# Kernel optimization log

Hardware: AMD Instinct MI355X
Metric: run time of the kernel (lower is better)

The kernel has to match this reference:

```python
import jax, jax.numpy as jnp
import numpy as np

BS, N, XC, K, YS = 64, 1024, 1024, 256, 768

def setup_inputs() -> dict:
    key = jax.random.key(0)
    ks = jax.random.split(key, 5)
    return {
        "x": jax.random.normal(ks[0], (BS, N, XC), dtype=jnp.float32),
        "y": jax.random.normal(ks[1], (BS, YS), dtype=jnp.float32),
        "W_ch": jax.random.normal(ks[2], (K, XC), dtype=jnp.float32) * 0.02,
        "b_ch": jax.random.normal(ks[3], (K,), dtype=jnp.float32) * 0.02,
        "W_y": jax.random.normal(ks[4], (K, YS), dtype=jnp.float32) * 0.02,
    }

def reference(x, y, W_ch, b_ch, W_y):
    # y_k: [bs, k] (no bias)
    y_k = jnp.einsum('bs,ks->bk', y, W_y)
    # channel affine on every spatial position, batched: [bs, n, k]
    x_k = jnp.einsum('bnc,kc->bnk', x, W_ch) + b_ch
    # add per-sample y_k (broadcast over spatial dim), tanh, softmax over k
    z = jnp.tanh(x_k + y_k[:, None, :])
    attn = jax.nn.softmax(z, axis=-1)
    # torch.cat over dim=0 of per-sample [n, k] blocks -> [bs*n, k]
    return attn.reshape(-1, attn.shape[-1])
```

## Files before the change

kernel.cpp:

```cpp
#include <hip/hip_runtime.h>


#define XC    1024
#define KOUT  256
#define NT    16
#define LDSZ  16384

typedef float        f32x4_t  __attribute__((ext_vector_type(4)));
typedef unsigned int u32x4_t  __attribute__((ext_vector_type(4)));
typedef unsigned int u32x2_t  __attribute__((ext_vector_type(2)));
typedef __bf16       bf16x8_t __attribute__((ext_vector_type(8)));

__device__ __forceinline__ unsigned short f2bf(float f) {
  unsigned int u = __float_as_uint(f);
  u += 0x7fffu + ((u >> 16) & 1u);
  return (unsigned short)(u >> 16);
}

__device__ __forceinline__ float fast_tanh(float v) {
  float e = __expf(2.0f * v);
  return 1.0f - 2.0f / (e + 1.0f);
}

#define LGKM_BARRIER() do {                                  \
    asm volatile("s_waitcnt lgkmcnt(0)" ::: "memory");       \
    __builtin_amdgcn_s_barrier();                            \
    __builtin_amdgcn_sched_barrier(0);                       \
  } while (0)

__global__ void prep_kernel(const float* __restrict__ Wch,
                            const float* __restrict__ y,
                            const float* __restrict__ Wy,
                            const float* __restrict__ bch,
                            unsigned short* __restrict__ wbf,
                            float* __restrict__ biasws) {
  if (blockIdx.x < 256) {
    const int k = blockIdx.x;
    const int u = threadIdx.x;
    f32x4_t v = ((const f32x4_t*)(Wch + k * XC))[u];
    const int c0   = u << 2;
    const int t    = c0 >> 6;
    const int ch   = (c0 & 63) >> 3;
    const int kk   = ch >> 2;
    const int lg   = ch & 3;
    const int half = (c0 >> 2) & 1;
    const int wv   = k >> 6;
    const int ni   = (k >> 4) & 3;
    const int lr   = k & 15;
    const int lane = (lg << 4) | lr;
    unsigned int lo = (unsigned int)f2bf(v.x) | ((unsigned int)f2bf(v.y) << 16);
    unsigned int hi = (unsigned int)f2bf(v.z) | ((unsigned int)f2bf(v.w) << 16);
    char* p = (char*)wbf +
              ((size_t)((((t << 2) + wv) * 2 + kk) * 4 + ni) << 10) +
              (lane << 4) + (half << 3);
    *(u32x2_t*)p = (u32x2_t){lo, hi};
  } else {
    __shared__ __align__(16) float ys[768];
    const int b = blockIdx.x - 256;
    const int k = threadIdx.x;
    for (int i = k; i < 768; i += 256) ys[i] = y[b * 768 + i];
    __syncthreads();
    const f32x4_t* w4 = (const f32x4_t*)(Wy + k * 768);
    const f32x4_t* y4 = (const f32x4_t*)ys;
    float s = 0.f;
#pragma unroll 8
    for (int i = 0; i < 192; ++i) {
      f32x4_t w = w4[i], a = y4[i];
      s = fmaf(w.x, a.x, s); s = fmaf(w.y, a.y, s);
      s = fmaf(w.z, a.z, s); s = fmaf(w.w, a.w, s);
    }
    biasws[b * 256 + k] = s + bch[k];
  }
}

__global__ __launch_bounds__(256, 2) void fused_kernel(
    const float* __restrict__ x, const unsigned short* __restrict__ wbf,
    const float* __restrict__ bias, float* __restrict__ out) {
  __shared__ __align__(16) unsigned char smem[LDSZ];
  const int tid = threadIdx.x;
  const int l   = tid & 63;
  const int wv  = tid >> 6;
  const int lr  = l & 15;
  const int lg  = l >> 4;
  const int m0  = blockIdx.x << 6;
  const int bidx = m0 >> 10;
  const int rr  = tid >> 4;
  const int c4  = tid & 15;
  const int t0  = blockIdx.x & 15;

  f32x4_t acc[4][4];
#pragma unroll
  for (int i = 0; i < 4; ++i)
#pragma unroll
    for (int j = 0; j < 4; ++j) acc[i][j] = (f32x4_t){0.f, 0.f, 0.f, 0.f};

  const float* xb = x + (size_t)m0 * XC + (size_t)rr * XC + (c4 << 2);
  const char* wsrc = (const char*)wbf + (wv << 13) + (l << 4);
  f32x4_t av0[4], av1[4], av2[4];
  bf16x8_t bfrA[8], bfrB[8];

#define LOADA(dst, tt) do {                                                  \
    _Pragma("unroll")                                                        \
    for (int j = 0; j < 4; ++j)                                              \
      dst[j] = *(const f32x4_t*)(xb + (size_t)(j << 4) * XC + ((tt) << 6));  \
  } while (0)

#define LOADB(dst, tt) do {                                                  \
    const char* g = wsrc + (size_t)(tt) * 32768;                             \
    _Pragma("unroll")                                                        \
    for (int f = 0; f < 8; ++f)                                              \
      dst[f] = __builtin_bit_cast(bf16x8_t, *(const u32x4_t*)(g + (f << 10)));\
  } while (0)

#define WRITEA(src, buf) do {                                                \
    _Pragma("unroll")                                                        \
    for (int j = 0; j < 4; ++j) {                                            \
      const int row = (j << 4) + rr;                                         \
      unsigned int lo = (unsigned int)f2bf(src[j].x) |                       \
                        ((unsigned int)f2bf(src[j].y) << 16);                \
      unsigned int hi = (unsigned int)f2bf(src[j].z) |                       \
                        ((unsigned int)f2bf(src[j].w) << 16);                \
      char* p = (char*)smem + ((buf) << 13) + row * 128 +                    \
                (((c4 >> 1) ^ (row & 7)) << 4) + ((c4 & 1) << 3);            \
      *(u32x2_t*)p = (u32x2_t){lo, hi};                                      \
    }                                                                        \
  } while (0)

#define COMPUTE(buf, bsrc) do {                                              \
    const u32x4_t* aB = (const u32x4_t*)(smem + ((buf) << 13));              \
    _Pragma("unroll")                                                        \
    for (int kk = 0; kk < 2; ++kk) {                                         \
      const int cs = ((kk << 2) | lg) ^ (lr & 7);                            \
      bf16x8_t afr[4];                                                       \
      _Pragma("unroll")                                                      \
      for (int mi = 0; mi < 4; ++mi)                                         \
        afr[mi] = __builtin_bit_cast(bf16x8_t, aB[(((mi << 4) + lr) << 3) + cs]);\
      _Pragma("unroll")                                                      \
      for (int mi = 0; mi < 4; ++mi)                                         \
        _Pragma("unroll")                                                    \
        for (int nj = 0; nj < 4; ++nj)                                       \
          acc[mi][nj] = __builtin_amdgcn_mfma_f32_16x16x32_bf16(             \
              afr[mi], bsrc[(kk << 2) | nj], acc[mi][nj], 0, 0, 0);          \
    }                                                                        \
  } while (0)

#define STEP(s, bC, bN, aW, aL, bufC, bufN) do {                             \
    if ((s) + 1 < NT) LOADB(bN, (((s) + 1 + t0) & 15));                      \
    if ((s) + 3 < NT) LOADA(aL, (((s) + 3 + t0) & 15));                      \
    COMPUTE(bufC, bC);                                                       \
    if ((s) + 1 < NT) { WRITEA(aW, bufN); LGKM_BARRIER(); }                  \
  } while (0)

  LOADB(bfrA, t0);
  LOADA(av0, t0);
  LOADA(av1, (t0 + 1) & 15);
  LOADA(av2, (t0 + 2) & 15);
  WRITEA(av0, 0);
  LGKM_BARRIER();

  STEP( 0, bfrA, bfrB, av1, av0, 0, 1);
  STEP( 1, bfrB, bfrA, av2, av1, 1, 0);
  STEP( 2, bfrA, bfrB, av0, av2, 0, 1);
  STEP( 3, bfrB, bfrA, av1, av0, 1, 0);
  STEP( 4, bfrA, bfrB, av2, av1, 0, 1);
  STEP( 5, bfrB, bfrA, av0, av2, 1, 0);
  STEP( 6, bfrA, bfrB, av1, av0, 0, 1);
  STEP( 7, bfrB, bfrA, av2, av1, 1, 0);
  STEP( 8, bfrA, bfrB, av0, av2, 0, 1);
  STEP( 9, bfrB, bfrA, av1, av0, 1, 0);
  STEP(10, bfrA, bfrB, av2, av1, 0, 1);
  STEP(11, bfrB, bfrA, av0, av2, 1, 0);
  STEP(12, bfrA, bfrB, av1, av0, 0, 1);
  STEP(13, bfrB, bfrA, av2, av1, 1, 0);
  STEP(14, bfrA, bfrB, av0, av2, 0, 1);
  STEP(15, bfrB, bfrA, av1, av0, 1, 0);

  __syncthreads();

#undef LOADA
#undef LOADB
#undef WRITEA
#undef COMPUTE
#undef STEP

  float* wred    = (float*)smem;
  float* rowstat = (float*)(smem + 1024);

  float brow[4];
#pragma unroll
  for (int ni = 0; ni < 4; ++ni)
    brow[ni] = bias[(bidx << 8) + (wv << 6) + (ni << 4) + lr];

#pragma unroll
  for (int mi = 0; mi < 4; ++mi)
#pragma unroll
    for (int ni = 0; ni < 4; ++ni)
#pragma unroll
      for (int r = 0; r < 4; ++r)
        acc[mi][ni][r] = fast_tanh(acc[mi][ni][r] + brow[ni]);

#pragma unroll
  for (int mi = 0; mi < 4; ++mi)
#pragma unroll
    for (int r = 0; r < 4; ++r) {
      float m = fmaxf(fmaxf(acc[mi][0][r], acc[mi][1][r]),
                      fmaxf(acc[mi][2][r], acc[mi][3][r]));
      m = fmaxf(m, __shfl_xor(m, 1));
      m = fmaxf(m, __shfl_xor(m, 2));
      m = fmaxf(m, __shfl_xor(m, 4));
      m = fmaxf(m, __shfl_xor(m, 8));
      if (lr == 0) wred[(wv << 6) + (mi << 4) + (lg << 2) + r] = m;
    }
  __syncthreads();
  if (tid < 64)
    rowstat[tid] = fmaxf(fmaxf(wred[tid], wred[64 + tid]),
                         fmaxf(wred[128 + tid], wred[192 + tid]));
  __syncthreads();

#pragma unroll
  for (int mi = 0; mi < 4; ++mi)
#pragma unroll
    for (int r = 0; r < 4; ++r) {
      const int row = (mi << 4) + (lg << 2) + r;
      const float m = rowstat[row];
      float s = 0.f;
#pragma unroll
      for (int ni = 0; ni < 4; ++ni) {
        float e = __expf(acc[mi][ni][r] - m);
        acc[mi][ni][r] = e;
        s += e;
      }
      s += __shfl_xor(s, 1);
      s += __shfl_xor(s, 2);
      s += __shfl_xor(s, 4);
      s += __shfl_xor(s, 8);
      if (lr == 0) wred[(wv << 6) + row] = s;
    }
  __syncthreads();
  if (tid < 64)
    rowstat[tid] = 1.0f / (wred[tid] + wred[64 + tid] +
                           wred[128 + tid] + wred[192 + tid]);
  __syncthreads();

#pragma unroll
  for (int mi = 0; mi < 4; ++mi)
#pragma unroll
    for (int r = 0; r < 4; ++r) {
      const int row = (mi << 4) + (lg << 2) + r;
      const float rinv = rowstat[row];
      float* orow = out + (size_t)(m0 + row) * KOUT + (wv << 6) + lr;
#pragma unroll
      for (int ni = 0; ni < 4; ++ni)
        orow[ni << 4] = acc[mi][ni][r] * rinv;
    }
}

extern "C" void kernel_launch(void* const* d_in, const int* in_sizes, int n_in,
                              void* d_out, int out_size, void* d_ws, size_t ws_size,
                              hipStream_t stream) {
  (void)in_sizes; (void)n_in; (void)out_size; (void)ws_size;
  const float* x   = (const float*)d_in[0];
  const float* y   = (const float*)d_in[1];
  const float* Wch = (const float*)d_in[2];
  const float* bch = (const float*)d_in[3];
  const float* Wy  = (const float*)d_in[4];
  float* out = (float*)d_out;
  unsigned short* wbf = (unsigned short*)d_ws;
  float* biasws = (float*)((char*)d_ws + 512 * 1024);

  hipLaunchKernelGGL(prep_kernel, dim3(320), dim3(256), 0, stream,
                     Wch, y, Wy, bch, wbf, biasws);
  hipLaunchKernelGGL(fused_kernel, dim3(1024), dim3(256), 0, stream,
                     x, wbf, biasws, out);
}
```

Before: 111.4 us.

## Process two row tiles per block, prefetching second tile during first

Halves the grid so each block computes two 64-row tiles back to back. The second tile's A and B loads are issued during the tail and epilogue of the first tile, which hides the pipeline fill latency. The bf16 conversion also moves to a cheaper pack with round-half-up instead of round-to-nearest-even. The cost is fewer blocks (512 on 256 CUs at 2 per CU), which may leave CUs underused, and higher register pressure from the prefetch held across the epilogue.

```diff
diff --git a/kernel.cpp b/kernel.cpp
--- a/kernel.cpp
+++ b/kernel.cpp
@@ -15,6 +15,12 @@
   unsigned int u = __float_as_uint(f);
   u += 0x7fffu + ((u >> 16) & 1u);
   return (unsigned short)(u >> 16);
+}
+
+__device__ __forceinline__ unsigned int pack2bf(float a, float b) {
+  unsigned int ua = __float_as_uint(a) + 0x8000u;
+  unsigned int ub = __float_as_uint(b) + 0x8000u;
+  return (ua >> 16) | (ub & 0xffff0000u);
 }
 
 __device__ __forceinline__ float fast_tanh(float v) {
@@ -82,27 +88,30 @@
   const int wv  = tid >> 6;
   const int lr  = l & 15;
   const int lg  = l >> 4;
-  const int m0  = blockIdx.x << 6;
-  const int bidx = m0 >> 10;
+  const int m0a = blockIdx.x << 6;
+  const int m0b = (blockIdx.x + 512) << 6;
   const int rr  = tid >> 4;
   const int c4  = tid & 15;
   const int t0  = blockIdx.x & 15;
 
   f32x4_t acc[4][4];
-#pragma unroll
-  for (int i = 0; i < 4; ++i)
-#pragma unroll
-    for (int j = 0; j < 4; ++j) acc[i][j] = (f32x4_t){0.f, 0.f, 0.f, 0.f};
-
-  const float* xb = x + (size_t)m0 * XC + (size_t)rr * XC + (c4 << 2);
+  const float* xb0 = x + (size_t)m0a * XC + (size_t)rr * XC + (c4 << 2);
+  const float* xb1 = x + (size_t)m0b * XC + (size_t)rr * XC + (c4 << 2);
   const char* wsrc = (const char*)wbf + (wv << 13) + (l << 4);
   f32x4_t av0[4], av1[4], av2[4];
   bf16x8_t bfrA[8], bfrB[8];
 
-#define LOADA(dst, tt) do {                                                  \
+#define ZERO_ACC() do {                                                      \
+    _Pragma("unroll")                                                        \
+    for (int i = 0; i < 4; ++i)                                              \
+      _Pragma("unroll")                                                      \
+      for (int j = 0; j < 4; ++j) acc[i][j] = (f32x4_t){0.f, 0.f, 0.f, 0.f}; \
+  } while (0)
+
+#define LOADA(dst, base, tt) do {                                            \
     _Pragma("unroll")                                                        \
     for (int j = 0; j < 4; ++j)                                              \
-      dst[j] = *(const f32x4_t*)(xb + (size_t)(j << 4) * XC + ((tt) << 6));  \
+      dst[j] = *(const f32x4_t*)((base) + (size_t)(j << 4) * XC + ((tt) << 6));\
   } while (0)
 
 #define LOADB(dst, tt) do {                                                  \
@@ -116,10 +125,8 @@
     _Pragma("unroll")                                                        \
     for (int j = 0; j < 4; ++j) {                                            \
       const int row = (j << 4) + rr;                                         \
-      unsigned int lo = (unsigned int)f2bf(src[j].x) |                       \
-                        ((unsigned int)f2bf(src[j].y) << 16);                \
-      unsigned int hi = (unsigned int)f2bf(src[j].z) |                       \
-                        ((unsigned int)f2bf(src[j].w) << 16);                \
+      unsigned int lo = pack2bf(src[j].x, src[j].y);                         \
+      unsigned int hi = pack2bf(src[j].z, src[j].w);                         \
       char* p = (char*)smem + ((buf) << 13) + row * 128 +                    \
                 (((c4 >> 1) ^ (row & 7)) << 4) + ((c4 & 1) << 3);            \
       *(u32x2_t*)p = (u32x2_t){lo, hi};                                      \
@@ -144,115 +151,158 @@
     }                                                                        \
   } while (0)
 
-#define STEP(s, bC, bN, aW, aL, bufC, bufN) do {                             \
-    if ((s) + 1 < NT) LOADB(bN, (((s) + 1 + t0) & 15));                      \
-    if ((s) + 3 < NT) LOADA(aL, (((s) + 3 + t0) & 15));                      \
-    COMPUTE(bufC, bC);                                                       \
-    if ((s) + 1 < NT) { WRITEA(aW, bufN); LGKM_BARRIER(); }                  \
-  } while (0)
-
+#define STEP(s, bC, bN, aW, aL, XB) do {                                     \
+    LOADB(bN, (((s) + 1 + t0) & 15));                                        \
+    LOADA(aL, XB, (((s) + 3 + t0) & 15));                                    \
+    COMPUTE((s) & 1, bC);                                                    \
+    WRITEA(aW, ((s) + 1) & 1);                                               \
+    LGKM_BARRIER();                                                          \
+  } while (0)
+
+#define EPILOGUE(M0V, BIDXV) do {                                            \
+    float* wred    = (float*)smem;                                           \
+    float* rowstat = (float*)(smem + 1024);                                  \
+    float brow[4];                                                           \
+    _Pragma("unroll")                                                        \
+    for (int ni = 0; ni < 4; ++ni)                                           \
+      brow[ni] = bias[((BIDXV) << 8) + (wv << 6) + (ni << 4) + lr];          \
+    _Pragma("unroll")                                                        \
+    for (int mi = 0; mi < 4; ++mi)                                           \
+      _Pragma("unroll")                                                      \
+      for (int ni = 0; ni < 4; ++ni)                                         \
+        _Pragma("unroll")                                                    \
+        for (int r = 0; r < 4; ++r)                                          \
+          acc[mi][ni][r] = fast_tanh(acc[mi][ni][r] + brow[ni]);             \
+    _Pragma("unroll")                                                        \
+    for (int mi = 0; mi < 4; ++mi)                                           \
+      _Pragma("unroll")                                                      \
+      for (int r = 0; r < 4; ++r) {                                          \
+        float m = fmaxf(fmaxf(acc[mi][0][r], acc[mi][1][r]),                 \
+                        fmaxf(acc[mi][2][r], acc[mi][3][r]));                \
+        m = fmaxf(m, __shfl_xor(m, 1));                                      \
+        m = fmaxf(m, __shfl_xor(m, 2));                                      \
+        m = fmaxf(m, __shfl_xor(m, 4));                                      \
+        m = fmaxf(m, __shfl_xor(m, 8));                                      \
+        if (lr == 0) wred[(wv << 6) + (mi << 4) + (lg << 2) + r] = m;        \
+      }                                                                      \
+    LGKM_BARRIER();                                                          \
+    if (tid < 64)                                                            \
+      rowstat[tid] = fmaxf(fmaxf(wred[tid], wred[64 + tid]),                 \
+                           fmaxf(wred[128 + tid], wred[192 + tid]));         \
+    LGKM_BARRIER();                                                          \
+    _Pragma("unroll")                                                        \
+    for (int mi = 0; mi < 4; ++mi)                                           \
+      _Pragma("unroll")                                                      \
+      for (int r = 0; r < 4; ++r) {                                          \
+        const int row = (mi << 4) + (lg << 2) + r;                           \
+        const float m = rowstat[row];                                        \
+        float s = 0.f;                                                       \
+        _Pragma("unroll")                                                    \
+        for (int ni = 0; ni < 4; ++ni) {                                     \
+          float e = __expf(acc[mi][ni][r] - m);                              \
+          acc[mi][ni][r] = e;                                                \
+          s += e;                                                            \
+        }                                                                    \
+        s += __shfl_xor(s, 1);                                               \
+        s += __shfl_xor(s, 2);                                               \
+        s += __shfl_xor(s, 4);                                               \
+        s += __shfl_xor(s, 8);                                               \
+        if (lr == 0) wred[(wv << 6) + row] = s;                              \
+      }                                                                      \
+    LGKM_BARRIER();                                                          \
+    if (tid < 64)                                                            \
+      rowstat[tid] = 1.0f / (wred[tid] + wred[64 + tid] +                    \
+                             wred[128 + tid] + wred[192 + tid]);             \
+    LGKM_BARRIER();                                                          \
+    _Pragma("unroll")                                                        \
+    for (int mi = 0; mi < 4; ++mi)                                           \
+      _Pragma("unroll")                                                      \
+      for (int r = 0; r < 4; ++r) {                                          \
+        const int row = (mi << 4) + (lg << 2) + r;                           \
+        const float rinv = rowstat[row];                                     \
+        float* orow = out + (size_t)((M0V) + row) * KOUT + (wv << 6) + lr;   \
+        _Pragma("unroll")                                                    \
+        for (int ni = 0; ni < 4; ++ni)                                       \
+          orow[ni << 4] = acc[mi][ni][r] * rinv;                             \
+      }                                                                      \
+  } while (0)
+
+  ZERO_ACC();
   LOADB(bfrA, t0);
-  LOADA(av0, t0);
-  LOADA(av1, (t0 + 1) & 15);
-  LOADA(av2, (t0 + 2) & 15);
+  LOADA(av0, xb0, t0);
+  LOADA(av1, xb0, (t0 + 1) & 15);
+  LOADA(av2, xb0, (t0 + 2) & 15);
   WRITEA(av0, 0);
   LGKM_BARRIER();
 
-  STEP( 0, bfrA, bfrB, av1, av0, 0, 1);
-  STEP( 1, bfrB, bfrA, av2, av1, 1, 0);
-  STEP( 2, bfrA, bfrB, av0, av2, 0, 1);
-  STEP( 3, bfrB, bfrA, av1, av0, 1, 0);
-  STEP( 4, bfrA, bfrB, av2, av1, 0, 1);
-  STEP( 5, bfrB, bfrA, av0, av2, 1, 0);
-  STEP( 6, bfrA, bfrB, av1, av0, 0, 1);
-  STEP( 7, bfrB, bfrA, av2, av1, 1, 0);
-  STEP( 8, bfrA, bfrB, av0, av2, 0, 1);
-  STEP( 9, bfrB, bfrA, av1, av0, 1, 0);
-  STEP(10, bfrA, bfrB, av2, av1, 0, 1);
-  STEP(11, bfrB, bfrA, av0, av2, 1, 0);
-  STEP(12, bfrA, bfrB, av1, av0, 0, 1);
-  STEP(13, bfrB, bfrA, av2, av1, 1, 0);
-  STEP(14, bfrA, bfrB, av0, av2, 0, 1);
-  STEP(15, bfrB, bfrA, av1, av0, 1, 0);
-
-  __syncthreads();
-
+  STEP( 0, bfrA, bfrB, av1, av0, xb0);
+  STEP( 1, bfrB, bfrA, av2, av1, xb0);
+  STEP( 2, bfrA, bfrB, av0, av2, xb0);
+  STEP( 3, bfrB, bfrA, av1, av0, xb0);
+  STEP( 4, bfrA, bfrB, av2, av1, xb0);
+  STEP( 5, bfrB, bfrA, av0, av2, xb0);
+  STEP( 6, bfrA, bfrB, av1, av0, xb0);
+  STEP( 7, bfrB, bfrA, av2, av1, xb0);
+  STEP( 8, bfrA, bfrB, av0, av2, xb0);
+  STEP( 9, bfrB, bfrA, av1, av0, xb0);
+  STEP(10, bfrA, bfrB, av2, av1, xb0);
+  STEP(11, bfrB, bfrA, av0, av2, xb0);
+  STEP(12, bfrA, bfrB, av1, av0, xb0);
+  LOADB(bfrA, (14 + t0) & 15);
+  LOADA(av1, xb1, t0);
+  COMPUTE(1, bfrB);
+  WRITEA(av2, 0);
+  LGKM_BARRIER();
+  LOADB(bfrB, (15 + t0) & 15);
+  LOADA(av2, xb1, (t0 + 1) & 15);
+  COMPUTE(0, bfrA);
+  WRITEA(av0, 1);
+  LGKM_BARRIER();
+  LOADB(bfrA, t0);
+  LOADA(av0, xb1, (t0 + 2) & 15);
+  COMPUTE(1, bfrB);
+  LGKM_BARRIER();
+
+  EPILOGUE(m0a, (m0a >> 10));
+  LGKM_BARRIER();
+
+  ZERO_ACC();
+  WRITEA(av1, 0);
+  LGKM_BARRIER();
+
+  STEP( 0, bfrA, bfrB, av2, av1, xb1);
+  STEP( 1, bfrB, bfrA, av0, av2, xb1);
+  STEP( 2, bfrA, bfrB, av1, av0, xb1);
+  STEP( 3, bfrB, bfrA, av2, av1, xb1);
+  STEP( 4, bfrA, bfrB, av0, av2, xb1);
+  STEP( 5, bfrB, bfrA, av1, av0, xb1);
+  STEP( 6, bfrA, bfrB, av2, av1, xb1);
+  STEP( 7, bfrB, bfrA, av0, av2, xb1);
+  STEP( 8, bfrA, bfrB, av1, av0, xb1);
+  STEP( 9, bfrB, bfrA, av2, av1, xb1);
+  STEP(10, bfrA, bfrB, av0, av2, xb1);
+  STEP(11, bfrB, bfrA, av1, av0, xb1);
+  STEP(12, bfrA, bfrB, av2, av1, xb1);
+  LOADB(bfrA, (14 + t0) & 15);
+  COMPUTE(1, bfrB);
+  WRITEA(av0, 0);
+  LGKM_BARRIER();
+  LOADB(bfrB, (15 + t0) & 15);
+  COMPUTE(0, bfrA);
+  WRITEA(av1, 1);
+  LGKM_BARRIER();
+  COMPUTE(1, bfrB);
+  LGKM_BARRIER();
+
+  EPILOGUE(m0b, (m0b >> 10));
+
+#undef ZERO_ACC
 #undef LOADA
 #undef LOADB
 #undef WRITEA
 #undef COMPUTE
 #undef STEP
-
-  float* wred    = (float*)smem;
-  float* rowstat = (float*)(smem + 1024);
-
-  float brow[4];
-#pragma unroll
-  for (int ni = 0; ni < 4; ++ni)
-    brow[ni] = bias[(bidx << 8) + (wv << 6) + (ni << 4) + lr];
-
-#pragma unroll
-  for (int mi = 0; mi < 4; ++mi)
-#pragma unroll
-    for (int ni = 0; ni < 4; ++ni)
-#pragma unroll
-      for (int r = 0; r < 4; ++r)
-        acc[mi][ni][r] = fast_tanh(acc[mi][ni][r] + brow[ni]);
-
-#pragma unroll
-  for (int mi = 0; mi < 4; ++mi)
-#pragma unroll
-    for (int r = 0; r < 4; ++r) {
-      float m = fmaxf(fmaxf(acc[mi][0][r], acc[mi][1][r]),
-                      fmaxf(acc[mi][2][r], acc[mi][3][r]));
-      m = fmaxf(m, __shfl_xor(m, 1));
-      m = fmaxf(m, __shfl_xor(m, 2));
-      m = fmaxf(m, __shfl_xor(m, 4));
-      m = fmaxf(m, __shfl_xor(m, 8));
-      if (lr == 0) wred[(wv << 6) + (mi << 4) + (lg << 2) + r] = m;
-    }
-  __syncthreads();
-  if (tid < 64)
-    rowstat[tid] = fmaxf(fmaxf(wred[tid], wred[64 + tid]),
-                         fmaxf(wred[128 + tid], wred[192 + tid]));
-  __syncthreads();
-
-#pragma unroll
-  for (int mi = 0; mi < 4; ++mi)
-#pragma unroll
-    for (int r = 0; r < 4; ++r) {
-      const int row = (mi << 4) + (lg << 2) + r;
-      const float m = rowstat[row];
-      float s = 0.f;
-#pragma unroll
-      for (int ni = 0; ni < 4; ++ni) {
-        float e = __expf(acc[mi][ni][r] - m);
-        acc[mi][ni][r] = e;
-        s += e;
-      }
-      s += __shfl_xor(s, 1);
-      s += __shfl_xor(s, 2);
-      s += __shfl_xor(s, 4);
-      s += __shfl_xor(s, 8);
-      if (lr == 0) wred[(wv << 6) + row] = s;
-    }
-  __syncthreads();
-  if (tid < 64)
-    rowstat[tid] = 1.0f / (wred[tid] + wred[64 + tid] +
-                           wred[128 + tid] + wred[192 + tid]);
-  __syncthreads();
-
-#pragma unroll
-  for (int mi = 0; mi < 4; ++mi)
-#pragma unroll
-    for (int r = 0; r < 4; ++r) {
-      const int row = (mi << 4) + (lg << 2) + r;
-      const float rinv = rowstat[row];
-      float* orow = out + (size_t)(m0 + row) * KOUT + (wv << 6) + lr;
-#pragma unroll
-      for (int ni = 0; ni < 4; ++ni)
-        orow[ni << 4] = acc[mi][ni][r] * rinv;
-    }
+#undef EPILOGUE
 }
 
 extern "C" void kernel_launch(void* const* d_in, const int* in_sizes, int n_in,
@@ -270,6 +320,6 @@
 
   hipLaunchKernelGGL(prep_kernel, dim3(320), dim3(256), 0, stream,
                      Wch, y, Wy, bch, wbf, biasws);
-  hipLaunchKernelGGL(fused_kernel, dim3(1024), dim3(256), 0, stream,
+  hipLaunchKernelGGL(fused_kernel, dim3(512), dim3(256), 0, stream,
                      x, wbf, biasws, out);
 }
```

New measurement: 132.8 us. 1.19x slower.
